# Performance work log

Hardware: AMD Instinct MI355X
Metric: run time of the kernel (lower is better)

The kernel has to match this reference:

```python
import jax, jax.numpy as jnp
import numpy as np

STATE_DIM = 1024
INPUT_DIM = 1024
BATCH = 8192


def setup_inputs() -> dict:
    key = jax.random.key(0)
    ks = jax.random.split(key, 7)
    # Kaiming-uniform-ish init like torch Linear
    bx = 1.0 / np.sqrt(INPUT_DIM)
    bh = 1.0 / np.sqrt(STATE_DIM)
    return {
        "x": jax.random.normal(ks[0], (BATCH, INPUT_DIM), jnp.float32),
        "prevh": jax.random.normal(ks[1], (BATCH, STATE_DIM), jnp.float32),
        "prevc": jax.random.normal(ks[2], (BATCH, STATE_DIM), jnp.float32),
        "Wx": jax.random.uniform(ks[3], (INPUT_DIM, 4 * STATE_DIM), jnp.float32, -bx, bx),
        "bx": jax.random.uniform(ks[4], (4 * STATE_DIM,), jnp.float32, -bx, bx),
        "Wh": jax.random.uniform(ks[5], (STATE_DIM, 4 * STATE_DIM), jnp.float32, -bh, bh),
    }


def reference(x, prevh, prevc, Wx, bx, Wh):
    # stacked gate pre-activations: [B, 4*state_dim]
    stacked = x @ Wx + bx + prevh @ Wh
    i_bar, f_bar, o_bar, g_bar = jnp.split(stacked, 4, axis=1)
    i = jax.nn.sigmoid(i_bar)
    f = jax.nn.sigmoid(f_bar)
    o = jax.nn.sigmoid(o_bar)
    g = jnp.tanh(g_bar)
    nextc = prevc * f + g * i
    nexth = jnp.tanh(nextc) * o
    return (nexth, nextc)
```

## Files before the change

### kernel.cpp

```cpp
#include <hip/hip_runtime.h>
#include <hip/hip_bf16.h>


#define BATCH   8192
#define SDIM    1024
#define KDIM    2048
#define NT      64

typedef __attribute__((ext_vector_type(8))) short s16x8;
typedef __attribute__((ext_vector_type(4))) float f32x4;

__device__ __forceinline__ void gload16(const void* g, void* l) {
    __builtin_amdgcn_global_load_lds((const __attribute__((address_space(1))) void*)g,
                                     (__attribute__((address_space(3))) void*)l,
                                     16, 0, 0);
}

__device__ __forceinline__ float fast_sigmoid(float x) {
    return 1.0f / (1.0f + __expf(-x));
}
__device__ __forceinline__ float fast_tanh(float v) {
    float a = fabsf(v);
    float e = __expf(-2.0f * a);
    float t = (1.0f - e) / (1.0f + e);
    return copysignf(t, v);
}

__global__ void convA(const float* __restrict__ x, const float* __restrict__ h,
                      __hip_bfloat16* __restrict__ A) {
    int t = blockIdx.x * blockDim.x + threadIdx.x;
    int e = t << 3;
    int b = e >> 11;
    int k = e & 2047;
    const float* src = (k < 1024) ? (x + (size_t)b * 1024 + k)
                                  : (h + (size_t)b * 1024 + (k - 1024));
    float4 v0 = *(const float4*)(src);
    float4 v1 = *(const float4*)(src + 4);
    union { __hip_bfloat16 b[8]; s16x8 v; } u;
    u.b[0] = __float2bfloat16(v0.x); u.b[1] = __float2bfloat16(v0.y);
    u.b[2] = __float2bfloat16(v0.z); u.b[3] = __float2bfloat16(v0.w);
    u.b[4] = __float2bfloat16(v1.x); u.b[5] = __float2bfloat16(v1.y);
    u.b[6] = __float2bfloat16(v1.z); u.b[7] = __float2bfloat16(v1.w);
    *(s16x8*)(A + e) = u.v;
}

__global__ void convW(const float* __restrict__ Wx, const float* __restrict__ Wh,
                      __hip_bfloat16* __restrict__ Wt) {
    __shared__ float tile[32][33];
    int k0 = blockIdx.x * 32;
    int n0 = blockIdx.y * 32;
    int tx = threadIdx.x;
    int ty = threadIdx.y;
#pragma unroll
    for (int j = 0; j < 4; ++j) {
        int k = k0 + ty + j * 8;
        int n = n0 + tx;
        float v = (k < 1024) ? Wx[(size_t)k * 4096 + n]
                             : Wh[(size_t)(k - 1024) * 4096 + n];
        tile[ty + j * 8][tx] = v;
    }
    __syncthreads();
#pragma unroll
    for (int j = 0; j < 4; ++j) {
        int n = n0 + ty + j * 8;
        int k = k0 + tx;
        int np = ((n & 1023) >> 4) * 64 + (n >> 10) * 16 + (n & 15);
        Wt[(size_t)np * 2048 + k] = __float2bfloat16(tile[tx][ty + j * 8]);
    }
}

__global__ __launch_bounds__(512, 2) void lstm_gemm(
    const __hip_bfloat16* __restrict__ A,
    const __hip_bfloat16* __restrict__ Wt,
    const float* __restrict__ bx,
    const float* __restrict__ prevc,
    float* __restrict__ outh,
    float* __restrict__ outc)
{
    __shared__ __align__(16) __hip_bfloat16 lds[4 * 16384];

    const int tid  = threadIdx.x;
    const int lane = tid & 63;
    const int w    = tid >> 6;
    const int wr   = w >> 2;
    const int wc   = w & 3;

    const int bid = blockIdx.x;
    const int swz = (bid & 7) * 64 + (bid >> 3);
    const int m0  = (swz & 31) * 256;
    const int nt  = swz >> 5;
    const int n0  = nt * 256;
    const int S0  = nt * 64;

    f32x4 acc[8][4];
#pragma unroll
    for (int m = 0; m < 8; ++m)
#pragma unroll
        for (int g = 0; g < 4; ++g)
            acc[m][g] = (f32x4)0.0f;

    const int srow = lane >> 2;
    const int scol = (((lane & 3) ^ ((lane >> 2) & 3)) << 3);
    const __hip_bfloat16* Ag = A  + (size_t)m0 * KDIM;
    const __hip_bfloat16* Bg = Wt + (size_t)n0 * KDIM;

    auto STAGE = [&](int t) {
        const int b  = (t & 3) * 16384;
        const int kt = t * 32;
#pragma unroll
        for (int r = 0; r < 2; ++r) {
            int row = r * 128 + w * 16 + srow;
            gload16(Ag + (size_t)row * KDIM + kt + scol,
                    &lds[b + r * 4096 + w * 512]);
        }
#pragma unroll
        for (int r = 0; r < 2; ++r) {
            int row = r * 128 + w * 16 + srow;
            gload16(Bg + (size_t)row * KDIM + kt + scol,
                    &lds[b + 8192 + r * 4096 + w * 512]);
        }
    };

    STAGE(0);
    STAGE(1);

    const int sslot = (((lane >> 4) ^ (lane & 3)) << 4);
    const int arow  = wr * 128 + (lane & 15);
    const int brow  = wc * 64  + (lane & 15);

    for (int t = 0; t < NT; ++t) {
        if (t + 2 < NT) {
            STAGE(t + 2);
            asm volatile("s_waitcnt vmcnt(8)" ::: "memory");
        } else if (t + 1 < NT) {
            asm volatile("s_waitcnt vmcnt(4)" ::: "memory");
        } else {
            asm volatile("s_waitcnt vmcnt(0)" ::: "memory");
        }
        __builtin_amdgcn_s_barrier();
        __builtin_amdgcn_sched_barrier(0);

        const char* base = (const char*)lds + (t & 3) * 32768;
        s16x8 af[8], bfr[4];
#pragma unroll
        for (int m = 0; m < 8; ++m)
            af[m] = *(const s16x8*)(base + (arow + m * 16) * 64 + sslot);
#pragma unroll
        for (int g = 0; g < 4; ++g)
            bfr[g] = *(const s16x8*)(base + 16384 + (brow + g * 16) * 64 + sslot);

        __builtin_amdgcn_s_setprio(1);
#pragma unroll
        for (int m = 0; m < 8; ++m)
#pragma unroll
            for (int g = 0; g < 4; ++g)
                acc[m][g] = __builtin_amdgcn_mfma_f32_16x16x32_bf16(
                    af[m], bfr[g], acc[m][g], 0, 0, 0);
        __builtin_amdgcn_s_setprio(0);
    }

    const int st  = S0 + wc * 16 + (lane & 15);
    const float b_i = bx[st];
    const float b_f = bx[1024 + st];
    const float b_o = bx[2048 + st];
    const float b_g = bx[3072 + st];
    const int rbase = m0 + wr * 128 + (lane >> 4) * 4;

#pragma unroll
    for (int m = 0; m < 8; ++m) {
#pragma unroll
        for (int q = 0; q < 4; ++q) {
            int row = rbase + m * 16 + q;
            float ib = acc[m][0][q] + b_i;
            float fb = acc[m][1][q] + b_f;
            float ob = acc[m][2][q] + b_o;
            float gb = acc[m][3][q] + b_g;
            float ig = fast_sigmoid(ib);
            float fg = fast_sigmoid(fb);
            float og = fast_sigmoid(ob);
            float gg = fast_tanh(gb);
            float pc = prevc[(size_t)row * SDIM + st];
            float nc = pc * fg + gg * ig;
            float nh = fast_tanh(nc) * og;
            outh[(size_t)row * SDIM + st] = nh;
            outc[(size_t)row * SDIM + st] = nc;
        }
    }
}

extern "C" void kernel_launch(void* const* d_in, const int* in_sizes, int n_in,
                              void* d_out, int out_size, void* d_ws, size_t ws_size,
                              hipStream_t stream) {
    const float* x     = (const float*)d_in[0];
    const float* prevh = (const float*)d_in[1];
    const float* prevc = (const float*)d_in[2];
    const float* Wx    = (const float*)d_in[3];
    const float* bx    = (const float*)d_in[4];
    const float* Wh    = (const float*)d_in[5];

    __hip_bfloat16* Abf = (__hip_bfloat16*)d_ws;
    __hip_bfloat16* Wt  = Abf + (size_t)BATCH * KDIM;

    float* outh = (float*)d_out;
    float* outc = outh + (size_t)BATCH * SDIM;

    hipLaunchKernelGGL(convA, dim3(8192), dim3(256), 0, stream, x, prevh, Abf);
    hipLaunchKernelGGL(convW, dim3(64, 128), dim3(32, 8), 0, stream, Wx, Wh, Wt);
    hipLaunchKernelGGL(lstm_gemm, dim3(512), dim3(512), 0, stream,
                       Abf, Wt, bx, prevc, outh, outc);
}
```

Baseline: 175.0 us.

## Restructure GEMM main loop into 4-phase ping-pong with K=64 tiles

Doubles the K-tile to 64 (halving loop iterations) and splits each iteration into four phases. Each phase interleaves LDS fragment reads, staged global-to-LDS loads of half-tiles for the next iterations, and a quarter of the MFMA work, separated by barriers. It also changes the LDS swizzle to suit 128-byte rows and remaps blocks to tiles so each XCD handles an 8x8 patch of tiles. The aim is better overlap of memory and compute and better L2 locality, at the cost of 128KB LDS per block (likely one block per CU) and more barriers.

```diff
diff --git a/kernel.cpp b/kernel.cpp
--- a/kernel.cpp
+++ b/kernel.cpp
@@ -5,7 +5,7 @@
 #define BATCH   8192
 #define SDIM    1024
 #define KDIM    2048
-#define NT      64
+#define NT      32
 
 typedef __attribute__((ext_vector_type(8))) short s16x8;
 typedef __attribute__((ext_vector_type(4))) float f32x4;
@@ -77,20 +77,39 @@
     float* __restrict__ outh,
     float* __restrict__ outc)
 {
-    __shared__ __align__(16) __hip_bfloat16 lds[4 * 16384];
+    __shared__ __align__(16) char lds[131072];
 
     const int tid  = threadIdx.x;
     const int lane = tid & 63;
     const int w    = tid >> 6;
     const int wr   = w >> 2;
     const int wc   = w & 3;
+    const int l15  = lane & 15;
 
     const int bid = blockIdx.x;
-    const int swz = (bid & 7) * 64 + (bid >> 3);
-    const int m0  = (swz & 31) * 256;
-    const int nt  = swz >> 5;
-    const int n0  = nt * 256;
-    const int S0  = nt * 64;
+    const int xcd = bid & 7, j = bid >> 3;
+    const int mt = (xcd >> 1) * 8 + (j & 7);
+    const int nt = (xcd & 1) * 8 + (j >> 3);
+    const int m0 = mt * 256, n0 = nt * 256, S0 = nt * 64;
+
+    const int scol = ((lane & 7) ^ (lane >> 3)) << 3;
+    const __hip_bfloat16* Ag = A  + (size_t)m0 * KDIM;
+    const __hip_bfloat16* Bg = Wt + (size_t)n0 * KDIM;
+
+    auto SA = [&](int tt, int p) {
+        char* dst = lds + (2 * (tt & 1) + p) * 16384 + w * 1024;
+        const __hip_bfloat16* src =
+            Ag + (size_t)(p * 128 + w * 8 + (lane >> 3)) * KDIM + tt * 64 + scol;
+        gload16(src, dst);
+        gload16(src + (size_t)64 * KDIM, dst + 8192);
+    };
+    auto SB = [&](int tt, int p) {
+        char* dst = lds + 65536 + (2 * (tt & 1) + p) * 16384 + w * 1024;
+        const __hip_bfloat16* src =
+            Bg + (size_t)(p * 128 + w * 8 + (lane >> 3)) * KDIM + tt * 64 + scol;
+        gload16(src, dst);
+        gload16(src + (size_t)64 * KDIM, dst + 8192);
+    };
 
     f32x4 acc[8][4];
 #pragma unroll
@@ -99,67 +118,105 @@
         for (int g = 0; g < 4; ++g)
             acc[m][g] = (f32x4)0.0f;
 
-    const int srow = lane >> 2;
-    const int scol = (((lane & 3) ^ ((lane >> 2) & 3)) << 3);
-    const __hip_bfloat16* Ag = A  + (size_t)m0 * KDIM;
-    const __hip_bfloat16* Bg = Wt + (size_t)n0 * KDIM;
-
-    auto STAGE = [&](int t) {
-        const int b  = (t & 3) * 16384;
-        const int kt = t * 32;
-#pragma unroll
-        for (int r = 0; r < 2; ++r) {
-            int row = r * 128 + w * 16 + srow;
-            gload16(Ag + (size_t)row * KDIM + kt + scol,
-                    &lds[b + r * 4096 + w * 512]);
-        }
-#pragma unroll
-        for (int r = 0; r < 2; ++r) {
-            int row = r * 128 + w * 16 + srow;
-            gload16(Bg + (size_t)row * KDIM + kt + scol,
-                    &lds[b + 8192 + r * 4096 + w * 512]);
-        }
-    };
-
-    STAGE(0);
-    STAGE(1);
-
-    const int sslot = (((lane >> 4) ^ (lane & 3)) << 4);
-    const int arow  = wr * 128 + (lane & 15);
-    const int brow  = wc * 64  + (lane & 15);
+    SB(0, 0); SB(0, 1); SA(0, 0); SA(0, 1); SB(1, 0); SB(1, 1);
+    asm volatile("s_waitcnt vmcnt(4)" ::: "memory");
+    __builtin_amdgcn_s_barrier();
+
+    const int swz0 = (((lane >> 4))     ^ (lane & 7)) << 4;
+    const int swz1 = (((lane >> 4) | 4) ^ (lane & 7)) << 4;
+    const int brow = (wc & 1) * 64;
+
+    s16x8 af[4][2], bf[4][2];
+
+#define PH_SYNC()                                           \
+    __builtin_amdgcn_s_barrier();                           \
+    asm volatile("s_waitcnt lgkmcnt(0)" ::: "memory");      \
+    __builtin_amdgcn_sched_barrier(0);                      \
+    __builtin_amdgcn_s_setprio(1);
+
+#define PH_END()                                            \
+    __builtin_amdgcn_s_setprio(0);                          \
+    __builtin_amdgcn_s_barrier();
 
     for (int t = 0; t < NT; ++t) {
+        const char* as = lds + (2 * (t & 1) + wr) * 16384;
+        const char* bs = lds + 65536 + (2 * (t & 1) + (wc >> 1)) * 16384;
+
+#pragma unroll
+        for (int m = 0; m < 4; ++m) {
+            af[m][0] = *(const s16x8*)(as + (m * 16 + l15) * 128 + swz0);
+            af[m][1] = *(const s16x8*)(as + (m * 16 + l15) * 128 + swz1);
+        }
+#pragma unroll
+        for (int g = 0; g < 2; ++g) {
+            bf[g][0] = *(const s16x8*)(bs + (brow + g * 16 + l15) * 128 + swz0);
+            bf[g][1] = *(const s16x8*)(bs + (brow + g * 16 + l15) * 128 + swz1);
+        }
+        if (t + 1 < NT) SA(t + 1, 0);
+        PH_SYNC();
+#pragma unroll
+        for (int m = 0; m < 4; ++m)
+#pragma unroll
+            for (int g = 0; g < 2; ++g) {
+                acc[m][g] = __builtin_amdgcn_mfma_f32_16x16x32_bf16(af[m][0], bf[g][0], acc[m][g], 0, 0, 0);
+                acc[m][g] = __builtin_amdgcn_mfma_f32_16x16x32_bf16(af[m][1], bf[g][1], acc[m][g], 0, 0, 0);
+            }
+        PH_END();
+
+#pragma unroll
+        for (int g = 2; g < 4; ++g) {
+            bf[g][0] = *(const s16x8*)(bs + (brow + g * 16 + l15) * 128 + swz0);
+            bf[g][1] = *(const s16x8*)(bs + (brow + g * 16 + l15) * 128 + swz1);
+        }
+        if (t + 1 < NT) SA(t + 1, 1);
+        PH_SYNC();
+#pragma unroll
+        for (int m = 0; m < 4; ++m)
+#pragma unroll
+            for (int g = 2; g < 4; ++g) {
+                acc[m][g] = __builtin_amdgcn_mfma_f32_16x16x32_bf16(af[m][0], bf[g][0], acc[m][g], 0, 0, 0);
+                acc[m][g] = __builtin_amdgcn_mfma_f32_16x16x32_bf16(af[m][1], bf[g][1], acc[m][g], 0, 0, 0);
+            }
+        PH_END();
+
+#pragma unroll
+        for (int m = 0; m < 4; ++m) {
+            af[m][0] = *(const s16x8*)(as + ((m + 4) * 16 + l15) * 128 + swz0);
+            af[m][1] = *(const s16x8*)(as + ((m + 4) * 16 + l15) * 128 + swz1);
+        }
+        if (t + 2 < NT) SB(t + 2, 0);
+        PH_SYNC();
+#pragma unroll
+        for (int m = 0; m < 4; ++m)
+#pragma unroll
+            for (int g = 2; g < 4; ++g) {
+                acc[m + 4][g] = __builtin_amdgcn_mfma_f32_16x16x32_bf16(af[m][0], bf[g][0], acc[m + 4][g], 0, 0, 0);
+                acc[m + 4][g] = __builtin_amdgcn_mfma_f32_16x16x32_bf16(af[m][1], bf[g][1], acc[m + 4][g], 0, 0, 0);
+            }
+        PH_END();
+
+        if (t + 2 < NT) SB(t + 2, 1);
+        __builtin_amdgcn_s_barrier();
+        __builtin_amdgcn_s_setprio(1);
+#pragma unroll
+        for (int m = 0; m < 4; ++m)
+#pragma unroll
+            for (int g = 0; g < 2; ++g) {
+                acc[m + 4][g] = __builtin_amdgcn_mfma_f32_16x16x32_bf16(af[m][0], bf[g][0], acc[m + 4][g], 0, 0, 0);
+                acc[m + 4][g] = __builtin_amdgcn_mfma_f32_16x16x32_bf16(af[m][1], bf[g][1], acc[m + 4][g], 0, 0, 0);
+            }
+        __builtin_amdgcn_s_setprio(0);
         if (t + 2 < NT) {
-            STAGE(t + 2);
-            asm volatile("s_waitcnt vmcnt(8)" ::: "memory");
-        } else if (t + 1 < NT) {
             asm volatile("s_waitcnt vmcnt(4)" ::: "memory");
         } else {
             asm volatile("s_waitcnt vmcnt(0)" ::: "memory");
         }
         __builtin_amdgcn_s_barrier();
-        __builtin_amdgcn_sched_barrier(0);
-
-        const char* base = (const char*)lds + (t & 3) * 32768;
-        s16x8 af[8], bfr[4];
-#pragma unroll
-        for (int m = 0; m < 8; ++m)
-            af[m] = *(const s16x8*)(base + (arow + m * 16) * 64 + sslot);
-#pragma unroll
-        for (int g = 0; g < 4; ++g)
-            bfr[g] = *(const s16x8*)(base + 16384 + (brow + g * 16) * 64 + sslot);
-
-        __builtin_amdgcn_s_setprio(1);
-#pragma unroll
-        for (int m = 0; m < 8; ++m)
-#pragma unroll
-            for (int g = 0; g < 4; ++g)
-                acc[m][g] = __builtin_amdgcn_mfma_f32_16x16x32_bf16(
-                    af[m], bfr[g], acc[m][g], 0, 0, 0);
-        __builtin_amdgcn_s_setprio(0);
-    }
-
-    const int st  = S0 + wc * 16 + (lane & 15);
+    }
+#undef PH_SYNC
+#undef PH_END
+
+    const int st  = S0 + wc * 16 + l15;
     const float b_i = bx[st];
     const float b_f = bx[1024 + st];
     const float b_o = bx[2048 + st];
```

New measurement: 160.7 us. 8.2% less time.

## Switch LSTM GEMM to 32x32x16 MFMA with BK=64 double-buffered pipeline

Applied to the files above, without the earlier changes.

Replaces the 16x16x32 MFMA tiling with 32x32x16 MFMA tiles: each wave now computes 64x128 instead of 128x64, K-step grows to 64 with two LDS buffers, and the weight permutation groups gates in 32-column blocks. Fragment reads from LDS are interleaved with MFMAs using explicit lgkmcnt waits, and the block-to-tile mapping is reworked so tiles sharing A or B rows land on the same XCD. The goal is fewer LDS reads per FLOP and better latency hiding. The cost is a full vmcnt(0) barrier on every iteration and 128KB of LDS per block, which may limit occupancy to one block per CU.

```diff
diff --git a/kernel.cpp b/kernel.cpp
--- a/kernel.cpp
+++ b/kernel.cpp
@@ -5,10 +5,10 @@
 #define BATCH   8192
 #define SDIM    1024
 #define KDIM    2048
-#define NT      64
-
-typedef __attribute__((ext_vector_type(8))) short s16x8;
-typedef __attribute__((ext_vector_type(4))) float f32x4;
+#define NT      32
+
+typedef __attribute__((ext_vector_type(8)))  short s16x8;
+typedef __attribute__((ext_vector_type(16))) float f32x16;
 
 __device__ __forceinline__ void gload16(const void* g, void* l) {
     __builtin_amdgcn_global_load_lds((const __attribute__((address_space(1))) void*)g,
@@ -64,7 +64,7 @@
     for (int j = 0; j < 4; ++j) {
         int n = n0 + ty + j * 8;
         int k = k0 + tx;
-        int np = ((n & 1023) >> 4) * 64 + (n >> 10) * 16 + (n & 15);
+        int np = ((n & 1023) >> 5) * 128 + (n >> 10) * 32 + (n & 31);
         Wt[(size_t)np * 2048 + k] = __float2bfloat16(tile[tx][ty + j * 8]);
     }
 }
@@ -77,104 +77,124 @@
     float* __restrict__ outh,
     float* __restrict__ outc)
 {
-    __shared__ __align__(16) __hip_bfloat16 lds[4 * 16384];
+    __shared__ __align__(16) char lds[131072];
 
     const int tid  = threadIdx.x;
     const int lane = tid & 63;
     const int w    = tid >> 6;
-    const int wr   = w >> 2;
-    const int wc   = w & 3;
+    const int wv   = w >> 1;
+    const int wc   = w & 1;
+    const int l31  = lane & 31;
 
     const int bid = blockIdx.x;
-    const int swz = (bid & 7) * 64 + (bid >> 3);
-    const int m0  = (swz & 31) * 256;
-    const int nt  = swz >> 5;
-    const int n0  = nt * 256;
-    const int S0  = nt * 64;
-
-    f32x4 acc[8][4];
-#pragma unroll
-    for (int m = 0; m < 8; ++m)
-#pragma unroll
-        for (int g = 0; g < 4; ++g)
-            acc[m][g] = (f32x4)0.0f;
-
-    const int srow = lane >> 2;
-    const int scol = (((lane & 3) ^ ((lane >> 2) & 3)) << 3);
+    const int xcd = bid & 7, jj = bid >> 3;
+    const int mt = (xcd >> 1) * 8 + (jj & 7);
+    const int nt = (xcd & 1) * 8 + (jj >> 3);
+    const int m0 = mt * 256, n0 = nt * 256;
+
+    const int scol = ((lane & 7) ^ (lane >> 3)) << 3;
     const __hip_bfloat16* Ag = A  + (size_t)m0 * KDIM;
     const __hip_bfloat16* Bg = Wt + (size_t)n0 * KDIM;
 
-    auto STAGE = [&](int t) {
-        const int b  = (t & 3) * 16384;
-        const int kt = t * 32;
-#pragma unroll
-        for (int r = 0; r < 2; ++r) {
-            int row = r * 128 + w * 16 + srow;
-            gload16(Ag + (size_t)row * KDIM + kt + scol,
-                    &lds[b + r * 4096 + w * 512]);
-        }
-#pragma unroll
-        for (int r = 0; r < 2; ++r) {
-            int row = r * 128 + w * 16 + srow;
-            gload16(Bg + (size_t)row * KDIM + kt + scol,
-                    &lds[b + 8192 + r * 4096 + w * 512]);
-        }
+    auto SA = [&](int tt) {
+        char* dst = lds + (tt & 1) * 32768 + w * 1024;
+        const __hip_bfloat16* src =
+            Ag + (size_t)(w * 8 + (lane >> 3)) * KDIM + tt * 64 + scol;
+#pragma unroll
+        for (int r = 0; r < 4; ++r)
+            gload16(src + (size_t)(r * 64) * KDIM, dst + r * 8192);
     };
-
-    STAGE(0);
-    STAGE(1);
-
-    const int sslot = (((lane >> 4) ^ (lane & 3)) << 4);
-    const int arow  = wr * 128 + (lane & 15);
-    const int brow  = wc * 64  + (lane & 15);
+    auto SB = [&](int tt) {
+        char* dst = lds + 65536 + (tt & 1) * 32768 + w * 1024;
+        const __hip_bfloat16* src =
+            Bg + (size_t)(w * 8 + (lane >> 3)) * KDIM + tt * 64 + scol;
+#pragma unroll
+        for (int r = 0; r < 4; ++r)
+            gload16(src + (size_t)(r * 64) * KDIM, dst + r * 8192);
+    };
+
+    f32x16 acc[2][4];
+#pragma unroll
+    for (int m = 0; m < 2; ++m)
+#pragma unroll
+        for (int g = 0; g < 4; ++g)
+            acc[m][g] = (f32x16)0.0f;
+
+    SA(0); SB(0);
+    asm volatile("s_waitcnt vmcnt(0)" ::: "memory");
+    __builtin_amdgcn_s_barrier();
+    __builtin_amdgcn_sched_barrier(0);
+
+    int swzk[4];
+#pragma unroll
+    for (int ks = 0; ks < 4; ++ks)
+        swzk[ks] = (((ks * 2 + (lane >> 5)) ^ (lane & 7)) << 4);
+    const int arow = (wv * 64 + l31) * 128;
+    const int brow = (wc * 128 + l31) * 128;
+
+    s16x8 aP[2], bP[4], aQ[2], bQ[4];
+
+#define LGKM(n)                                             \
+    asm volatile("s_waitcnt lgkmcnt(" #n ")" ::: "memory"); \
+    __builtin_amdgcn_sched_barrier(0);
+
+#define RDC(AF, BF, KS)                                                       \
+    _Pragma("unroll")                                                         \
+    for (int m = 0; m < 2; ++m)                                               \
+        AF[m] = *(const s16x8*)(as + arow + m * 4096 + swzk[KS]);             \
+    _Pragma("unroll")                                                         \
+    for (int g = 0; g < 4; ++g)                                               \
+        BF[g] = *(const s16x8*)(bs + brow + g * 4096 + swzk[KS]);
+
+#define MC(AF, BF)                                                            \
+    __builtin_amdgcn_s_setprio(1);                                            \
+    _Pragma("unroll")                                                         \
+    for (int m = 0; m < 2; ++m)                                               \
+        _Pragma("unroll")                                                     \
+        for (int g = 0; g < 4; ++g)                                           \
+            acc[m][g] = __builtin_amdgcn_mfma_f32_32x32x16_bf16(              \
+                AF[m], BF[g], acc[m][g], 0, 0, 0);                            \
+    __builtin_amdgcn_s_setprio(0);
 
     for (int t = 0; t < NT; ++t) {
-        if (t + 2 < NT) {
-            STAGE(t + 2);
-            asm volatile("s_waitcnt vmcnt(8)" ::: "memory");
-        } else if (t + 1 < NT) {
-            asm volatile("s_waitcnt vmcnt(4)" ::: "memory");
-        } else {
-            asm volatile("s_waitcnt vmcnt(0)" ::: "memory");
-        }
+        const char* as = lds + (t & 1) * 32768;
+        const char* bs = lds + 65536 + (t & 1) * 32768;
+
+        if (t + 1 < NT) { SA(t + 1); SB(t + 1); }
+
+        RDC(aP, bP, 0);
+        RDC(aQ, bQ, 1);
+        LGKM(6);  MC(aP, bP);
+        RDC(aP, bP, 2);
+        LGKM(6);  MC(aQ, bQ);
+        RDC(aQ, bQ, 3);
+        LGKM(6);  MC(aP, bP);
+        LGKM(0);  MC(aQ, bQ);
+
+        asm volatile("s_waitcnt vmcnt(0)" ::: "memory");
         __builtin_amdgcn_s_barrier();
         __builtin_amdgcn_sched_barrier(0);
-
-        const char* base = (const char*)lds + (t & 3) * 32768;
-        s16x8 af[8], bfr[4];
-#pragma unroll
-        for (int m = 0; m < 8; ++m)
-            af[m] = *(const s16x8*)(base + (arow + m * 16) * 64 + sslot);
-#pragma unroll
-        for (int g = 0; g < 4; ++g)
-            bfr[g] = *(const s16x8*)(base + 16384 + (brow + g * 16) * 64 + sslot);
-
-        __builtin_amdgcn_s_setprio(1);
-#pragma unroll
-        for (int m = 0; m < 8; ++m)
-#pragma unroll
-            for (int g = 0; g < 4; ++g)
-                acc[m][g] = __builtin_amdgcn_mfma_f32_16x16x32_bf16(
-                    af[m], bfr[g], acc[m][g], 0, 0, 0);
-        __builtin_amdgcn_s_setprio(0);
-    }
-
-    const int st  = S0 + wc * 16 + (lane & 15);
+    }
+#undef RDC
+#undef MC
+#undef LGKM
+
+    const int st  = (nt * 2 + wc) * 32 + l31;
     const float b_i = bx[st];
     const float b_f = bx[1024 + st];
     const float b_o = bx[2048 + st];
     const float b_g = bx[3072 + st];
-    const int rbase = m0 + wr * 128 + (lane >> 4) * 4;
-
-#pragma unroll
-    for (int m = 0; m < 8; ++m) {
-#pragma unroll
-        for (int q = 0; q < 4; ++q) {
-            int row = rbase + m * 16 + q;
-            float ib = acc[m][0][q] + b_i;
-            float fb = acc[m][1][q] + b_f;
-            float ob = acc[m][2][q] + b_o;
-            float gb = acc[m][3][q] + b_g;
+    const int rbase = m0 + wv * 64 + ((lane >> 5) << 2);
+
+#pragma unroll
+    for (int m = 0; m < 2; ++m) {
+#pragma unroll
+        for (int reg = 0; reg < 16; ++reg) {
+            int row = rbase + m * 32 + (reg & 3) + ((reg >> 2) << 3);
+            float ib = acc[m][0][reg] + b_i;
+            float fb = acc[m][1][reg] + b_f;
+            float ob = acc[m][2][reg] + b_o;
+            float gb = acc[m][3][reg] + b_g;
             float ig = fast_sigmoid(ib);
             float fg = fast_sigmoid(fb);
             float og = fast_sigmoid(ob);
```

New measurement: 172.2 us. Within noise of the previous version (-1.6%).
